# Kernel optimization log

Hardware: AMD Instinct MI355X
Metric: run time of the kernel (lower is better)

The kernel has to match this reference:

```python
import jax, jax.numpy as jnp
import numpy as np

D_IN = 4096
NUM_LATENTS = 65536
GROUP_DIM = 64
GROUP_MUL = 4
IN_GROUPS = D_IN // GROUP_DIM      # 64
OUT_GROUPS = NUM_LATENTS // GROUP_DIM  # 1024
TOKENS = 2048


def setup_inputs() -> dict:
    key = jax.random.key(0)
    k1, k2, k3, k4, k5 = jax.random.split(key, 5)
    x = jax.random.normal(k1, (TOKENS, D_IN), dtype=jnp.float32)
    # nn.Linear default init ~ U(-1/sqrt(d), 1/sqrt(d)); scale randn similarly for stability
    s = 1.0 / np.sqrt(D_IN)
    pre_w = jax.random.normal(k2, (D_IN, D_IN), dtype=jnp.float32) * s
    pre_b = jax.random.normal(k3, (D_IN,), dtype=jnp.float32) * s
    inner = jax.random.normal(k4, (GROUP_MUL, IN_GROUPS, GROUP_DIM, GROUP_DIM), dtype=jnp.float32)
    outer = jax.random.normal(k5, (OUT_GROUPS, GROUP_MUL, IN_GROUPS), dtype=jnp.float32)
    return {"x": x, "pre_w": pre_w, "pre_b": pre_b, "inner": inner, "outer": outer}


def reference(x, pre_w, pre_b, inner, outer):
    # pre: dense linear, x @ W^T + b  -> (tokens, d_in)
    h = x @ pre_w.T + pre_b
    # unflatten last dim into (in_groups, group_dim)
    h = h.reshape(h.shape[0], IN_GROUPS, GROUP_DIM)  # (b, i, x)
    # block-diagonal mix: (b,i,x) x (m,i,x,y) -> (b,m,i,y)
    t = jnp.einsum('bix,mixy->bmiy', h, inner)
    # low-rank outer combine: (b,m,i,y) x (o,m,i) -> (b,o,y)
    out = jnp.einsum('bmiy,omi->boy', t, outer)
    # flatten (o, y) -> num_latents; note: module's _bias is unused in forward
    return out.reshape(out.shape[0], NUM_LATENTS)
```

## Files before the change

kernel.cpp:

```cpp
#include <hip/hip_runtime.h>
#include <hip/hip_bf16.h>
#include <stdint.h>

#define D_IN 4096
#define TOKENS 2048
#define NUM_LATENTS 65536
#define GROUP_DIM 64
#define GROUP_MUL 4
#define IN_GROUPS 64
#define OUT_GROUPS 1024
#define KMID 256

typedef __attribute__((ext_vector_type(8))) short short8;
typedef __attribute__((ext_vector_type(4))) float f32x4;

struct alignas(8)  US4 { unsigned short v[4]; };
struct alignas(16) US8 { unsigned short v[8]; };

__device__ inline unsigned short f2bf(float f) {
    union { float f; unsigned u; } w{f};
    unsigned r = w.u + 0x7fffu + ((w.u >> 16) & 1u);
    return (unsigned short)(r >> 16);
}

__device__ inline void gload_lds16(const void* g, void* l) {
    __builtin_amdgcn_global_load_lds(
        (const __attribute__((address_space(1))) void*)g,
        (__attribute__((address_space(3))) void*)l, 16, 0, 0);
}

__device__ inline int SWZ(int y, int k) {
    return ((y << 9) + (k << 1)) ^ (((y >> 3) & 7) << 4);
}

__global__ void cvt_all(const float* __restrict__ w, const float* __restrict__ x,
                        const float* __restrict__ outer,
                        unsigned short* __restrict__ w_bf, unsigned short* __restrict__ x_bf,
                        unsigned short* __restrict__ o_bf) {
    int s = blockIdx.x * blockDim.x + threadIdx.x;
    if (s < 4194304) {
        f32x4 v = *(const f32x4*)(w + (size_t)s * 4);
        US4 o;
        #pragma unroll
        for (int j = 0; j < 4; ++j) o.v[j] = f2bf(v[j]);
        *(US4*)(w_bf + (size_t)s * 4) = o;
    } else if (s < 6291456) {
        int t = s - 4194304;
        f32x4 v = *(const f32x4*)(x + (size_t)t * 4);
        US4 o;
        #pragma unroll
        for (int j = 0; j < 4; ++j) o.v[j] = f2bf(v[j]);
        *(US4*)(x_bf + (size_t)t * 4) = o;
    } else if (s < 6356992) {
        int t0 = (s - 6291456) * 4;
        int o = t0 >> 8, r = t0 & 255, m = r >> 6, i = r & 63;
        f32x4 v = *(const f32x4*)(outer + t0);
        #pragma unroll
        for (int j = 0; j < 4; ++j)
            o_bf[(o << 8) + (i + j) * 4 + m] = f2bf(v[j]);
    }
}

__global__ __launch_bounds__(256) void cvt_inner(const float* __restrict__ s, unsigned short* __restrict__ d) {
    __shared__ float tl[64][65];
    const int blk = blockIdx.x;
    const int tid = threadIdx.x;
    const float* src = s + (size_t)blk * 4096;
    #pragma unroll
    for (int p = 0; p < 4; ++p) {
        int idx = p * 1024 + tid * 4;
        int x = idx >> 6, y = idx & 63;
        f32x4 v = *(const f32x4*)(src + idx);
        #pragma unroll
        for (int j = 0; j < 4; ++j) tl[x][y + j] = v[j];
    }
    __syncthreads();
    unsigned short* dst = d + (size_t)blk * 4096;
    #pragma unroll
    for (int p = 0; p < 4; ++p) {
        int idx = p * 1024 + tid * 4;
        int y = idx >> 6, x0 = idx & 63;
        US4 o;
        #pragma unroll
        for (int j = 0; j < 4; ++j) o.v[j] = f2bf(tl[x0 + j][y]);
        *(US4*)(dst + y * 64 + (x0 ^ ((y & 7) << 3))) = o;
    }
}

__global__ __launch_bounds__(256) void gemm_fused(
    const unsigned short* __restrict__ A,
    const unsigned short* __restrict__ B,
    const float* __restrict__ bias,
    const unsigned short* __restrict__ IT,
    unsigned short* __restrict__ T)
{
    __shared__ unsigned short smem[24576];
    unsigned short* As = smem;
    unsigned short* Bs = smem + 8192;
    unsigned short* inn = smem + 16384;

    const int tid = threadIdx.x;
    const int lane = tid & 63;
    const int w = tid >> 6;
    const int wm = w >> 1, wn = w & 1;
    int bx = blockIdx.x;
    bx = (bx & 7) * 64 + (bx >> 3);
    const int m0 = (bx & 15) * 128;
    const int n0 = (bx >> 4) * 128;
    const int i0 = n0 >> 6;

    const int lr = lane & 15;
    const int lk = (lane >> 4) * 8;
    const int rin = (lane >> 4) * 4;

    f32x4 acc[4][4] = {};

    for (int k0 = 0; k0 < D_IN; k0 += 64) {
        #pragma unroll
        for (int c = 0; c < 4; ++c) {
            int f = c * 2048 + tid * 8;
            int r = f >> 6, col = f & 63;
            gload_lds16(A + (size_t)(m0 + r) * D_IN + k0 + col, As + f);
            gload_lds16(B + (size_t)(n0 + r) * D_IN + k0 + col, Bs + f);
        }
        asm volatile("s_waitcnt vmcnt(0)" ::: "memory");
        __syncthreads();
        #pragma unroll
        for (int kk = 0; kk < 2; ++kk) {
            short8 a[4], b[4];
            #pragma unroll
            for (int mi = 0; mi < 4; ++mi)
                a[mi] = *(const short8*)(As + (wm * 64 + mi * 16 + lr) * 64 + kk * 32 + lk);
            #pragma unroll
            for (int ni = 0; ni < 4; ++ni)
                b[ni] = *(const short8*)(Bs + (wn * 64 + ni * 16 + lr) * 64 + kk * 32 + lk);
            #pragma unroll
            for (int mi = 0; mi < 4; ++mi)
                #pragma unroll
                for (int ni = 0; ni < 4; ++ni)
                    acc[mi][ni] = __builtin_amdgcn_mfma_f32_16x16x32_bf16(a[mi], b[ni], acc[mi][ni], 0, 0, 0);
        }
        __syncthreads();
    }

    #pragma unroll
    for (int ni = 0; ni < 4; ++ni) {
        int col = wn * 64 + ni * 16 + lr;
        float bv = bias[n0 + col];
        #pragma unroll
        for (int mi = 0; mi < 4; ++mi) {
            #pragma unroll
            for (int j = 0; j < 4; ++j) {
                int tok = wm * 64 + mi * 16 + rin + j;
                smem[tok * 128 + (col ^ ((tok & 7) << 3))] = f2bf(acc[mi][ni][j] + bv);
            }
        }
    }

    for (int m = 0; m < 4; ++m) {
        #pragma unroll
        for (int c = 0; c < 4; ++c) {
            int e = c * 2048 + tid * 8;
            int i_loc = e >> 12, rem = e & 4095;
            gload_lds16(IT + ((size_t)(m * 64 + i0 + i_loc) << 12) + rem, inn + e);
        }
        asm volatile("s_waitcnt vmcnt(0)" ::: "memory");
        __syncthreads();

        f32x4 acc2[4][4] = {};
        #pragma unroll
        for (int kk = 0; kk < 2; ++kk) {
            short8 a[4], b2[4];
            #pragma unroll
            for (int mi = 0; mi < 4; ++mi) {
                int tok = wm * 64 + mi * 16 + lr;
                a[mi] = *(const short8*)(smem + tok * 128 + ((wn * 64 + kk * 32 + lk) ^ ((tok & 7) << 3)));
            }
            #pragma unroll
            for (int ni = 0; ni < 4; ++ni) {
                int y = ni * 16 + lr;
                b2[ni] = *(const short8*)(inn + wn * 4096 + y * 64 + ((kk * 32 + lk) ^ ((y & 7) << 3)));
            }
            #pragma unroll
            for (int mi = 0; mi < 4; ++mi)
                #pragma unroll
                for (int ni = 0; ni < 4; ++ni)
                    acc2[mi][ni] = __builtin_amdgcn_mfma_f32_16x16x32_bf16(a[mi], b2[ni], acc2[mi][ni], 0, 0, 0);
        }

        const int kp = (i0 + wn) * 4 + m;
        #pragma unroll
        for (int mi = 0; mi < 4; ++mi) {
            #pragma unroll
            for (int ni = 0; ni < 4; ++ni) {
                int y = ni * 16 + lr;
                #pragma unroll
                for (int j = 0; j < 4; ++j) {
                    int tok = m0 + wm * 64 + mi * 16 + rin + j;
                    T[((size_t)tok * KMID + kp) * 64 + y] = f2bf(acc2[mi][ni][j]);
                }
            }
        }
        __syncthreads();
    }
}

__global__ __launch_bounds__(512) void stage3(
    const unsigned short* __restrict__ T,
    const unsigned short* __restrict__ Ob,
    float* __restrict__ out)
{
    __shared__ char ts[32768];
    const int tid = threadIdx.x;
    const int lane = tid & 63;
    const int w = tid >> 6;
    int bx = blockIdx.x;
    const int b = (bx & 7) * 256 + (bx >> 3);
    const int lr = lane & 15;
    const int hi = lane >> 4;

    {
        const unsigned short* src = T + (size_t)b * (KMID * 64);
        #pragma unroll
        for (int c = 0; c < 4; ++c) {
            int e = c * 4096 + tid * 8;
            int k = e >> 6, y = e & 63;
            US8 v = *(const US8*)(src + e);
            #pragma unroll
            for (int j = 0; j < 8; ++j)
                *(unsigned short*)(ts + SWZ(y + j, k)) = v.v[j];
        }
    }
    __syncthreads();

    const int o_base = w * 128;
    f32x4 acc[4][8] = {};
    for (int kt = 0; kt < 8; ++kt) {
        short8 tf[4], of[8];
        #pragma unroll
        for (int ni = 0; ni < 4; ++ni)
            tf[ni] = *(const short8*)(ts + SWZ(ni * 16 + lr, kt * 32 + hi * 8));
        #pragma unroll
        for (int mi = 0; mi < 8; ++mi)
            of[mi] = *(const short8*)(Ob + ((size_t)(o_base + mi * 16 + lr) << 8) + kt * 32 + hi * 8);
        #pragma unroll
        for (int ni = 0; ni < 4; ++ni)
            #pragma unroll
            for (int mi = 0; mi < 8; ++mi)
                acc[ni][mi] = __builtin_amdgcn_mfma_f32_16x16x32_bf16(tf[ni], of[mi], acc[ni][mi], 0, 0, 0);
    }

    float* ob = out + (size_t)b * NUM_LATENTS;
    #pragma unroll
    for (int ni = 0; ni < 4; ++ni) {
        #pragma unroll
        for (int mi = 0; mi < 8; ++mi) {
            int o = o_base + mi * 16 + lr;
            int y = ni * 16 + hi * 4;
            *(f32x4*)(ob + (o << 6) + y) = acc[ni][mi];
        }
    }
}

extern "C" void kernel_launch(void* const* d_in, const int* in_sizes, int n_in,
                              void* d_out, int out_size, void* d_ws, size_t ws_size,
                              hipStream_t stream) {
    const float* x     = (const float*)d_in[0];
    const float* pre_w = (const float*)d_in[1];
    const float* pre_b = (const float*)d_in[2];
    const float* inner = (const float*)d_in[3];
    const float* outer = (const float*)d_in[4];
    float* out = (float*)d_out;

    char* ws = (char*)d_ws;
    unsigned short* x_bf = (unsigned short*)ws;  ws += (size_t)TOKENS * D_IN * 2;
    unsigned short* w_bf = (unsigned short*)ws;  ws += (size_t)D_IN * D_IN * 2;
    unsigned short* o_bf = (unsigned short*)ws;  ws += (size_t)OUT_GROUPS * KMID * 2;
    unsigned short* t_bf = (unsigned short*)ws;  ws += (size_t)TOKENS * KMID * 64 * 2;
    unsigned short* it_bf = (unsigned short*)ws; ws += (size_t)GROUP_MUL * IN_GROUPS * 64 * 64 * 2;

    cvt_all<<<(6356992 + 255) / 256, 256, 0, stream>>>(pre_w, x, outer, w_bf, x_bf, o_bf);
    cvt_inner<<<GROUP_MUL * IN_GROUPS, 256, 0, stream>>>(inner, it_bf);

    gemm_fused<<<512, 256, 0, stream>>>(x_bf, w_bf, pre_b, it_bf, t_bf);
    stage3<<<2048, 512, 0, stream>>>(t_bf, o_bf, out);
}
```

Baseline: 381.6 us.

## Double-buffer GEMM K loop, merge conversion kernels, vectorize stores, nontemporal I/O

Merges the inner-weight transpose conversion into the flat conversion kernel, removing one launch. The main GEMM now double-buffers its A/B LDS tiles, issuing the next tile's global-to-LDS loads before computing the current one, with partial vmcnt waits and raw barriers. MFMA operands are swapped so each lane holds contiguous columns, which lets the bias add and the epilogue stores to LDS and T use 4-wide packed writes instead of scalar ones. Stage3 uses nontemporal loads and stores for T and the output. LDS use grows to 80KB per block, which can reduce occupancy despite the launch_bounds hint.

```diff
diff --git a/kernel.cpp b/kernel.cpp
--- a/kernel.cpp
+++ b/kernel.cpp
@@ -15,7 +15,8 @@
 typedef __attribute__((ext_vector_type(4))) float f32x4;
 
 struct alignas(8)  US4 { unsigned short v[4]; };
-struct alignas(16) US8 { unsigned short v[8]; };
+
+#define FLAT_BLOCKS 24832
 
 __device__ inline unsigned short f2bf(float f) {
     union { float f; unsigned u; } w{f};
@@ -33,11 +34,39 @@
     return ((y << 9) + (k << 1)) ^ (((y >> 3) & 7) << 4);
 }
 
-__global__ void cvt_all(const float* __restrict__ w, const float* __restrict__ x,
-                        const float* __restrict__ outer,
-                        unsigned short* __restrict__ w_bf, unsigned short* __restrict__ x_bf,
-                        unsigned short* __restrict__ o_bf) {
-    int s = blockIdx.x * blockDim.x + threadIdx.x;
+__global__ __launch_bounds__(256) void cvt_all(
+    const float* __restrict__ w, const float* __restrict__ x,
+    const float* __restrict__ outer, const float* __restrict__ inner,
+    unsigned short* __restrict__ w_bf, unsigned short* __restrict__ x_bf,
+    unsigned short* __restrict__ o_bf, unsigned short* __restrict__ it_bf) {
+    __shared__ float tl[64][65];
+    int blk = blockIdx.x;
+    const int tid = threadIdx.x;
+    if (blk >= FLAT_BLOCKS) {
+        blk -= FLAT_BLOCKS;
+        const float* src = inner + (size_t)blk * 4096;
+        #pragma unroll
+        for (int p = 0; p < 4; ++p) {
+            int idx = p * 1024 + tid * 4;
+            int xx = idx >> 6, y = idx & 63;
+            f32x4 v = *(const f32x4*)(src + idx);
+            #pragma unroll
+            for (int j = 0; j < 4; ++j) tl[xx][y + j] = v[j];
+        }
+        __syncthreads();
+        unsigned short* dst = it_bf + (size_t)blk * 4096;
+        #pragma unroll
+        for (int p = 0; p < 4; ++p) {
+            int idx = p * 1024 + tid * 4;
+            int y = idx >> 6, x0 = idx & 63;
+            US4 o;
+            #pragma unroll
+            for (int j = 0; j < 4; ++j) o.v[j] = f2bf(tl[x0 + j][y]);
+            *(US4*)(dst + y * 64 + (x0 ^ ((y & 7) << 3))) = o;
+        }
+        return;
+    }
+    int s = blk * 256 + tid;
     if (s < 4194304) {
         f32x4 v = *(const f32x4*)(w + (size_t)s * 4);
         US4 o;
@@ -51,7 +80,7 @@
         #pragma unroll
         for (int j = 0; j < 4; ++j) o.v[j] = f2bf(v[j]);
         *(US4*)(x_bf + (size_t)t * 4) = o;
-    } else if (s < 6356992) {
+    } else {
         int t0 = (s - 6291456) * 4;
         int o = t0 >> 8, r = t0 & 255, m = r >> 6, i = r & 63;
         f32x4 v = *(const f32x4*)(outer + t0);
@@ -61,43 +90,15 @@
     }
 }
 
-__global__ __launch_bounds__(256) void cvt_inner(const float* __restrict__ s, unsigned short* __restrict__ d) {
-    __shared__ float tl[64][65];
-    const int blk = blockIdx.x;
-    const int tid = threadIdx.x;
-    const float* src = s + (size_t)blk * 4096;
-    #pragma unroll
-    for (int p = 0; p < 4; ++p) {
-        int idx = p * 1024 + tid * 4;
-        int x = idx >> 6, y = idx & 63;
-        f32x4 v = *(const f32x4*)(src + idx);
-        #pragma unroll
-        for (int j = 0; j < 4; ++j) tl[x][y + j] = v[j];
-    }
-    __syncthreads();
-    unsigned short* dst = d + (size_t)blk * 4096;
-    #pragma unroll
-    for (int p = 0; p < 4; ++p) {
-        int idx = p * 1024 + tid * 4;
-        int y = idx >> 6, x0 = idx & 63;
-        US4 o;
-        #pragma unroll
-        for (int j = 0; j < 4; ++j) o.v[j] = f2bf(tl[x0 + j][y]);
-        *(US4*)(dst + y * 64 + (x0 ^ ((y & 7) << 3))) = o;
-    }
-}
-
-__global__ __launch_bounds__(256) void gemm_fused(
+__global__ __launch_bounds__(256, 2) void gemm_fused(
     const unsigned short* __restrict__ A,
     const unsigned short* __restrict__ B,
     const float* __restrict__ bias,
     const unsigned short* __restrict__ IT,
     unsigned short* __restrict__ T)
 {
-    __shared__ unsigned short smem[24576];
-    unsigned short* As = smem;
-    unsigned short* Bs = smem + 8192;
-    unsigned short* inn = smem + 16384;
+    __shared__ unsigned short smem[40960];
+    unsigned short* inn = smem + 32768;
 
     const int tid = threadIdx.x;
     const int lane = tid & 63;
@@ -110,50 +111,67 @@
     const int i0 = n0 >> 6;
 
     const int lr = lane & 15;
-    const int lk = (lane >> 4) * 8;
-    const int rin = (lane >> 4) * 4;
+    const int hi = lane >> 4;
+    const int lk = hi * 8;
 
     f32x4 acc[4][4] = {};
 
-    for (int k0 = 0; k0 < D_IN; k0 += 64) {
+    auto STAGE = [&](int buf, int k0) {
         #pragma unroll
         for (int c = 0; c < 4; ++c) {
             int f = c * 2048 + tid * 8;
             int r = f >> 6, col = f & 63;
-            gload_lds16(A + (size_t)(m0 + r) * D_IN + k0 + col, As + f);
-            gload_lds16(B + (size_t)(n0 + r) * D_IN + k0 + col, Bs + f);
-        }
-        asm volatile("s_waitcnt vmcnt(0)" ::: "memory");
-        __syncthreads();
+            gload_lds16(A + (size_t)(m0 + r) * D_IN + k0 + col, smem + buf * 16384 + f);
+            gload_lds16(B + (size_t)(n0 + r) * D_IN + k0 + col, smem + buf * 16384 + 8192 + f);
+        }
+    };
+    auto COMPUTE = [&](int buf) {
+        const unsigned short* as = smem + buf * 16384;
+        const unsigned short* bs = as + 8192;
         #pragma unroll
         for (int kk = 0; kk < 2; ++kk) {
             short8 a[4], b[4];
             #pragma unroll
             for (int mi = 0; mi < 4; ++mi)
-                a[mi] = *(const short8*)(As + (wm * 64 + mi * 16 + lr) * 64 + kk * 32 + lk);
+                a[mi] = *(const short8*)(as + (wm * 64 + mi * 16 + lr) * 64 + kk * 32 + lk);
             #pragma unroll
             for (int ni = 0; ni < 4; ++ni)
-                b[ni] = *(const short8*)(Bs + (wn * 64 + ni * 16 + lr) * 64 + kk * 32 + lk);
+                b[ni] = *(const short8*)(bs + (wn * 64 + ni * 16 + lr) * 64 + kk * 32 + lk);
             #pragma unroll
             for (int mi = 0; mi < 4; ++mi)
                 #pragma unroll
                 for (int ni = 0; ni < 4; ++ni)
-                    acc[mi][ni] = __builtin_amdgcn_mfma_f32_16x16x32_bf16(a[mi], b[ni], acc[mi][ni], 0, 0, 0);
-        }
-        __syncthreads();
-    }
+                    acc[mi][ni] = __builtin_amdgcn_mfma_f32_16x16x32_bf16(b[ni], a[mi], acc[mi][ni], 0, 0, 0);
+        }
+    };
+
+    STAGE(0, 0);
+    #pragma unroll 1
+    for (int t = 0; t < 63; ++t) {
+        STAGE((t + 1) & 1, (t + 1) * 64);
+        asm volatile("s_waitcnt vmcnt(8)" ::: "memory");
+        __builtin_amdgcn_s_barrier();
+        __builtin_amdgcn_sched_barrier(0);
+        COMPUTE(t & 1);
+        __builtin_amdgcn_s_barrier();
+        __builtin_amdgcn_sched_barrier(0);
+    }
+    asm volatile("s_waitcnt vmcnt(0)" ::: "memory");
+    __builtin_amdgcn_s_barrier();
+    __builtin_amdgcn_sched_barrier(0);
+    COMPUTE(1);
 
     #pragma unroll
     for (int ni = 0; ni < 4; ++ni) {
-        int col = wn * 64 + ni * 16 + lr;
-        float bv = bias[n0 + col];
+        int col0 = wn * 64 + ni * 16 + hi * 4;
+        f32x4 bv = *(const f32x4*)(bias + n0 + col0);
         #pragma unroll
         for (int mi = 0; mi < 4; ++mi) {
-            #pragma unroll
-            for (int j = 0; j < 4; ++j) {
-                int tok = wm * 64 + mi * 16 + rin + j;
-                smem[tok * 128 + (col ^ ((tok & 7) << 3))] = f2bf(acc[mi][ni][j] + bv);
-            }
+            int tok = wm * 64 + mi * 16 + lr;
+            US4 o;
+            #pragma unroll
+            for (int j = 0; j < 4; ++j) o.v[j] = f2bf(acc[mi][ni][j] + bv[j]);
+            *(US4*)(smem + tok * 128 + (col0 ^ ((tok & 7) << 3))) = o;
         }
     }
 
@@ -185,20 +203,21 @@
             for (int mi = 0; mi < 4; ++mi)
                 #pragma unroll
                 for (int ni = 0; ni < 4; ++ni)
-                    acc2[mi][ni] = __builtin_amdgcn_mfma_f32_16x16x32_bf16(a[mi], b2[ni], acc2[mi][ni], 0, 0, 0);
+                    acc2[mi][ni] = __builtin_amdgcn_mfma_f32_16x16x32_bf16(b2[ni], a[mi], acc2[mi][ni], 0, 0, 0);
         }
 
         const int kp = (i0 + wn) * 4 + m;
         #pragma unroll
         for (int mi = 0; mi < 4; ++mi) {
+            int tok = m0 + wm * 64 + mi * 16 + lr;
+            unsigned short* trow = T + ((size_t)tok * KMID + kp) * 64;
             #pragma unroll
             for (int ni = 0; ni < 4; ++ni) {
-                int y = ni * 16 + lr;
+                int y0 = ni * 16 + hi * 4;
+                US4 o;
                 #pragma unroll
-                for (int j = 0; j < 4; ++j) {
-                    int tok = m0 + wm * 64 + mi * 16 + rin + j;
-                    T[((size_t)tok * KMID + kp) * 64 + y] = f2bf(acc2[mi][ni][j]);
-                }
+                for (int j = 0; j < 4; ++j) o.v[j] = f2bf(acc2[mi][ni][j]);
+                *(US4*)(trow + y0) = o;
             }
         }
         __syncthreads();
@@ -225,10 +244,10 @@
         for (int c = 0; c < 4; ++c) {
             int e = c * 4096 + tid * 8;
             int k = e >> 6, y = e & 63;
-            US8 v = *(const US8*)(src + e);
+            short8 v = __builtin_nontemporal_load((const short8*)(src + e));
             #pragma unroll
             for (int j = 0; j < 8; ++j)
-                *(unsigned short*)(ts + SWZ(y + j, k)) = v.v[j];
+                *(unsigned short*)(ts + SWZ(y + j, k)) = (unsigned short)v[j];
         }
     }
     __syncthreads();
@@ -257,7 +276,7 @@
         for (int mi = 0; mi < 8; ++mi) {
             int o = o_base + mi * 16 + lr;
             int y = ni * 16 + hi * 4;
-            *(f32x4*)(ob + (o << 6) + y) = acc[ni][mi];
+            __builtin_nontemporal_store(acc[ni][mi], (f32x4*)(ob + (o << 6) + y));
         }
     }
 }
@@ -279,8 +298,8 @@
     unsigned short* t_bf = (unsigned short*)ws;  ws += (size_t)TOKENS * KMID * 64 * 2;
     unsigned short* it_bf = (unsigned short*)ws; ws += (size_t)GROUP_MUL * IN_GROUPS * 64 * 64 * 2;
 
-    cvt_all<<<(6356992 + 255) / 256, 256, 0, stream>>>(pre_w, x, outer, w_bf, x_bf, o_bf);
-    cvt_inner<<<GROUP_MUL * IN_GROUPS, 256, 0, stream>>>(inner, it_bf);
+    cvt_all<<<FLAT_BLOCKS + GROUP_MUL * IN_GROUPS, 256, 0, stream>>>(
+        pre_w, x, outer, inner, w_bf, x_bf, o_bf, it_bf);
 
     gemm_fused<<<512, 256, 0, stream>>>(x_bf, w_bf, pre_b, it_bf, t_bf);
     stage3<<<2048, 512, 0, stream>>>(t_bf, o_bf, out);
```

After: 327.1 us. -14.3%, faster.
